# Kernel tuning notes

Hardware: AMD Instinct MI355X
Metric: run time of the kernel (lower is better)

The kernel has to match this reference:

```python
import jax, jax.numpy as jnp
import numpy as np

B, S, D, H = 2, 2048, 2048, 16
DH = D // H
NEG = -1000000000.0


def setup_inputs() -> dict:
    key = jax.random.key(0)
    ks = jax.random.split(key, 5)
    return {
        "query_vector": jax.random.normal(ks[0], (B, S, D), dtype=jnp.float32),
        "key_vector": jax.random.normal(ks[1], (B, S, D), dtype=jnp.float32),
        "value_vector": jax.random.normal(ks[2], (B, S, D), dtype=jnp.float32),
        "W_qkv": jax.random.normal(ks[3], (D, 3 * D), dtype=jnp.float32) * (1.0 / np.sqrt(D)),
        "b_qkv": jax.random.normal(ks[4], (3 * D,), dtype=jnp.float32) * 0.01,
    }


def reference(query_vector, key_vector, value_vector, W_qkv, b_qkv):
    # NOTE: original forward only consumes query_vector; key/value args unused.
    qkv = query_vector @ W_qkv + b_qkv                      # [B, S, 3D]
    q, k, v = jnp.split(qkv, 3, axis=-1)                    # each [B, S, D]
    # Faithful to original: plain reshape (NOT transpose) into heads.
    q = q.reshape(B, H, S, DH)
    k = k.reshape(B, H, S, DH)
    v = v.reshape(B, H, S, DH)
    scores = jnp.einsum("bhqd,bhkd->bhqk", q, k) / np.float32(np.sqrt(DH))
    # torch.triu_indices(offset=0): mask j >= i (diagonal included), SET to -1e9.
    idx = jnp.arange(S)
    causal = idx[None, :] >= idx[:, None]                   # [S, S], True where masked
    scores = jnp.where(causal, jnp.float32(NEG), scores)
    attn = jax.nn.softmax(scores, axis=-1)
    out = jnp.einsum("bhqk,bhkd->bhqd", attn, v)            # [B, H, S, DH]
    # dropout is identity in eval mode
    return out.reshape(B, S, D)
```

## Files before the change

kernel.cpp:

```cpp
#include <hip/hip_runtime.h>
#include <hip/hip_bf16.h>
#include <stdint.h>

typedef unsigned short u16;
typedef short short8 __attribute__((ext_vector_type(8)));
typedef short short4v __attribute__((ext_vector_type(4)));
typedef float f32x4 __attribute__((ext_vector_type(4)));

#define CSL (0.08838834764831845f * 1.4426950408889634f)
#define NEGR -1.0e13f


__device__ __forceinline__ u16 f2b(float f) {
  union { float f; unsigned int u; } c; c.f = f;
  unsigned int u = c.u;
  u += 0x7fffu + ((u >> 16) & 1u);
  return (u16)(u >> 16);
}
__device__ __forceinline__ float b2f(u16 h) {
  union { float f; unsigned int u; } c; c.u = ((unsigned int)h) << 16;
  return c.f;
}

__global__ __launch_bounds__(256) void k_cast_q(const float* __restrict__ in, u16* __restrict__ out) {
  size_t idx = ((size_t)blockIdx.x * 256 + threadIdx.x) * 8;
  float4 f0 = *(const float4*)(in + idx);
  float4 f1 = *(const float4*)(in + idx + 4);
  short8 o;
  o[0] = (short)f2b(f0.x); o[1] = (short)f2b(f0.y); o[2] = (short)f2b(f0.z); o[3] = (short)f2b(f0.w);
  o[4] = (short)f2b(f1.x); o[5] = (short)f2b(f1.y); o[6] = (short)f2b(f1.z); o[7] = (short)f2b(f1.w);
  *(short8*)(out + idx) = o;
}

__global__ __launch_bounds__(256) void k_cast_wt(const float* __restrict__ W, u16* __restrict__ Wt) {
  __shared__ u16 L[64 * 68];
  const int t = threadIdx.x;
  const int nb = blockIdx.x * 64;
  const int kb = blockIdx.y * 64;
#pragma unroll
  for (int it = 0; it < 4; ++it) {
    int idx = it * 1024 + t * 4;
    int r = idx >> 6, c = idx & 63;
    float4 f = *(const float4*)(W + (size_t)(kb + r) * 6144 + nb + c);
    L[r * 68 + c + 0] = f2b(f.x);
    L[r * 68 + c + 1] = f2b(f.y);
    L[r * 68 + c + 2] = f2b(f.z);
    L[r * 68 + c + 3] = f2b(f.w);
  }
  __syncthreads();
#pragma unroll
  for (int it = 0; it < 4; ++it) {
    int idx = it * 1024 + t * 4;
    int i = idx >> 6, j = idx & 63;
    short4v o;
#pragma unroll
    for (int e = 0; e < 4; ++e) o[e] = (short)L[(j + e) * 68 + i];
    *(short4v*)(Wt + (size_t)(nb + i) * 2048 + kb + j) = o;
  }
}

__global__ __launch_bounds__(512, 1) void k_gemm256(const u16* __restrict__ A,
                                                    const u16* __restrict__ Bt,
                                                    const float* __restrict__ bias,
                                                    u16* __restrict__ qb,
                                                    u16* __restrict__ kbuf,
                                                    u16* __restrict__ vbuf) {
  __shared__ u16 As[2][16384];
  __shared__ u16 Bs[2][12288];
  const int t = threadIdx.x;
  const int ln = t & 63, w = t >> 6;
  const int lr = ln & 15, lg = ln >> 4;
  const int wm = w >> 2, wn = w & 3;
  const int Lid = blockIdx.x;
  const int xcd = Lid & 7, l = Lid >> 3;
  const int mt = (xcd & 1) * 8 + (l & 7);
  const int nt = (xcd >> 1) * 8 + (l >> 3);
  const int mb = mt * 256, nb = nt * 192;
  const int cswz = (lr & 7) * 8;
  const int srow = w * 8 + (ln >> 3);
  const int scol = ((ln & 7) ^ (ln >> 3)) * 8;

  const u16* Abase = A + (size_t)mb * 2048;
  const u16* Bbase = Bt + (size_t)nb * 2048;

  f32x4 acc[8][3] = {};

#define STAGE_KT(kt_, buf_)                                                                        \
  do {                                                                                             \
    const u16* as_ = Abase + (size_t)srow * 2048 + (kt_) * 64 + scol;                              \
    const u16* bs_ = Bbase + (size_t)srow * 2048 + (kt_) * 64 + scol;                              \
    _Pragma("unroll")                                                                              \
    for (int p = 0; p < 4; ++p)                                                                    \
      __builtin_amdgcn_global_load_lds(                                                            \
          (const __attribute__((address_space(1))) void*)(as_ + (size_t)p * 64 * 2048),            \
          (__attribute__((address_space(3))) void*)(&As[buf_][p * 4096 + w * 512]), 16, 0, 0);     \
    _Pragma("unroll")                                                                              \
    for (int p = 0; p < 3; ++p)                                                                    \
      __builtin_amdgcn_global_load_lds(                                                            \
          (const __attribute__((address_space(1))) void*)(bs_ + (size_t)p * 64 * 2048),            \
          (__attribute__((address_space(3))) void*)(&Bs[buf_][p * 4096 + w * 512]), 16, 0, 0);     \
  } while (0)

  STAGE_KT(0, 0);
  asm volatile("s_waitcnt vmcnt(0)" ::: "memory");
  __builtin_amdgcn_s_barrier();

  for (int kt = 0; kt < 32; ++kt) {
    const int cur = kt & 1;
    const u16* At = &As[cur][0];
    const u16* Bl = &Bs[cur][0];
    short8 af[4][2], bf[3][2];

#pragma unroll
    for (int mi = 0; mi < 4; ++mi)
#pragma unroll
      for (int ks = 0; ks < 2; ++ks)
        af[mi][ks] = *(const short8*)(At + (wm * 128 + mi * 16 + lr) * 64 + ((ks * 32 + lg * 8) ^ cswz));
#pragma unroll
    for (int ni = 0; ni < 3; ++ni)
#pragma unroll
      for (int ks = 0; ks < 2; ++ks)
        bf[ni][ks] = *(const short8*)(Bl + (wn * 48 + ni * 16 + lr) * 64 + ((ks * 32 + lg * 8) ^ cswz));
    if (kt + 1 < 32) STAGE_KT(kt + 1, cur ^ 1);
    __builtin_amdgcn_s_barrier();
    __builtin_amdgcn_s_setprio(1);
#pragma unroll
    for (int mi = 0; mi < 4; ++mi)
#pragma unroll
      for (int ni = 0; ni < 3; ++ni)
#pragma unroll
        for (int ks = 0; ks < 2; ++ks)
          acc[mi][ni] = __builtin_amdgcn_mfma_f32_16x16x32_bf16(af[mi][ks], bf[ni][ks], acc[mi][ni], 0, 0, 0);
    __builtin_amdgcn_s_setprio(0);
    __builtin_amdgcn_s_barrier();

#pragma unroll
    for (int mi = 0; mi < 4; ++mi)
#pragma unroll
      for (int ks = 0; ks < 2; ++ks)
        af[mi][ks] = *(const short8*)(At + (wm * 128 + 64 + mi * 16 + lr) * 64 + ((ks * 32 + lg * 8) ^ cswz));
    __builtin_amdgcn_s_barrier();
    __builtin_amdgcn_s_setprio(1);
#pragma unroll
    for (int mi = 0; mi < 4; ++mi)
#pragma unroll
      for (int ni = 0; ni < 3; ++ni)
#pragma unroll
        for (int ks = 0; ks < 2; ++ks)
          acc[4 + mi][ni] = __builtin_amdgcn_mfma_f32_16x16x32_bf16(af[mi][ks], bf[ni][ks], acc[4 + mi][ni], 0, 0, 0);
    __builtin_amdgcn_s_setprio(0);
    asm volatile("s_waitcnt vmcnt(0)" ::: "memory");
    __builtin_amdgcn_s_barrier();
  }
#undef STAGE_KT

#pragma unroll
  for (int ni = 0; ni < 3; ++ni) {
    int ncol = nb + wn * 48 + ni * 16 + lr;
    u16* dst = (ncol < 2048) ? qb : (ncol < 4096 ? kbuf : vbuf);
    int nmod = ncol & 2047;
    float bv = bias[ncol];
#pragma unroll
    for (int m = 0; m < 8; ++m) {
#pragma unroll
      for (int r = 0; r < 4; ++r) {
        int mrow = mb + wm * 128 + m * 16 + lg * 4 + r;
        dst[(size_t)mrow * 2048 + nmod] = f2b(acc[m][ni][r] + bv);
      }
    }
  }
}

__global__ __launch_bounds__(256) void k_vtrans(const u16* __restrict__ v, u16* __restrict__ vt,
                                                float* __restrict__ part) {
  __shared__ u16 L[128 * 136];
  __shared__ float Ls2[256];
  const int t = threadIdx.x;
  const int bh = blockIdx.y, sc = blockIdx.x;
  const size_t base = (size_t)bh * 262144;
#pragma unroll
  for (int it = 0; it < 8; ++it) {
    int chunk = it * 256 + t;
    int s = chunk >> 4, d8 = (chunk & 15) * 8;
    *(short8*)(L + s * 136 + d8) = *(const short8*)(v + base + (size_t)(sc * 128 + s) * 128 + d8);
  }
  __syncthreads();
#pragma unroll
  for (int it = 0; it < 8; ++it) {
    int chunk = it * 256 + t;
    int dh = chunk >> 4, s8 = (chunk & 15) * 8;
    short8 o;
#pragma unroll
    for (int e = 0; e < 8; ++e) o[e] = (short)L[(s8 + e) * 136 + dh];
    *(short8*)(vt + base + (size_t)dh * 2048 + sc * 128 + s8) = o;
  }
  {
    const int dh = t & 127, seg = t >> 7;
    float ps = 0.f;
#pragma unroll 8
    for (int i = 0; i < 64; ++i) ps += b2f(L[(seg * 64 + i) * 136 + dh]);
    Ls2[t] = ps;
    __syncthreads();
    if (t < 128) part[((size_t)bh * 16 + sc) * 128 + t] = Ls2[t] + Ls2[t + 128];
  }
}

__global__ __launch_bounds__(256, 3) void k_attn(const u16* __restrict__ qb,
                                                 const u16* __restrict__ kb,
                                                 const u16* __restrict__ vt,
                                                 const float* __restrict__ part,
                                                 float* __restrict__ out) {
  __shared__ u16 Ks[64 * 136];
  __shared__ u16 Vs[128 * 72];
  __shared__ u16 Ps[4][16 * 72];
  const int t = threadIdx.x;
  const int ln = t & 63, wv = t >> 6;
  const int lr = ln & 15, lg = ln >> 4;
  const int L = blockIdx.y * 32 + blockIdx.x;
  const int wl = (L & 7) * 128 + (L >> 3);
  const int bh = wl >> 5;
  const int qt = 31 - (wl & 31);
  const size_t base = (size_t)bh * 262144;
  const u16* Qh = qb + base;
  const u16* Kh = kb + base;
  const u16* Vth = vt + base;
  float* Oh = out + base;
  const int qs = qt * 64;

  short8 qf[4];
  {
    int qr = qs + wv * 16 + lr;
#pragma unroll
    for (int ks = 0; ks < 4; ++ks)
      qf[ks] = *(const short8*)(Qh + (size_t)qr * 128 + ks * 32 + lg * 8);
  }
  float lsum[4] = {0.f, 0.f, 0.f, 0.f};
  f32x4 acc[8];
  const f32x4 fz = {0.f, 0.f, 0.f, 0.f};
#pragma unroll
  for (int oj = 0; oj < 8; ++oj) acc[oj] = fz;

  u16* Pw = &Ps[wv][0];
  const int nkt = qt + 1;
  for (int kt = 0; kt < nkt; ++kt) {
#pragma unroll
    for (int it = 0; it < 4; ++it) {
      int chunk = it * 256 + t;
      int sk = chunk >> 4, d8 = (chunk & 15) * 8;
      *(short8*)(Ks + sk * 136 + d8) = *(const short8*)(Kh + (size_t)(kt * 64 + sk) * 128 + d8);
    }
#pragma unroll
    for (int it = 0; it < 4; ++it) {
      int chunk = it * 256 + t;
      int dh = chunk >> 3, s8 = (chunk & 7) * 8;
      *(short8*)(Vs + dh * 72 + s8) = *(const short8*)(Vth + (size_t)dh * 2048 + kt * 64 + s8);
    }
    __syncthreads();

    f32x4 s[4];
#pragma unroll
    for (int ni = 0; ni < 4; ++ni) s[ni] = fz;
#pragma unroll
    for (int ks = 0; ks < 4; ++ks) {
#pragma unroll
      for (int ni = 0; ni < 4; ++ni) {
        short8 kf = *(const short8*)(Ks + (ni * 16 + lr) * 136 + ks * 32 + lg * 8);
        s[ni] = __builtin_amdgcn_mfma_f32_16x16x32_bf16(qf[ks], kf, s[ni], 0, 0, 0);
      }
    }
    if (kt == qt) {
#pragma unroll
      for (int ni = 0; ni < 4; ++ni) {
        int col = kt * 64 + ni * 16 + lr;
#pragma unroll
        for (int r = 0; r < 4; ++r) {
          int row = qs + wv * 16 + lg * 4 + r;
          if (col >= row) s[ni][r] = NEGR;
        }
      }
    }
#pragma unroll
    for (int ni = 0; ni < 4; ++ni)
#pragma unroll
      for (int r = 0; r < 4; ++r) {
        u16 h = f2b(exp2f(s[ni][r] * CSL));
        Pw[(lg * 4 + r) * 72 + ni * 16 + lr] = h;
        lsum[r] += b2f(h);
      }
#pragma unroll
    for (int ks2 = 0; ks2 < 2; ++ks2) {
      short8 pa = *(const short8*)(Pw + lr * 72 + ks2 * 32 + lg * 8);
#pragma unroll
      for (int oj = 0; oj < 8; ++oj) {
        short8 vf = *(const short8*)(Vs + (oj * 16 + lr) * 72 + ks2 * 32 + lg * 8);
        acc[oj] = __builtin_amdgcn_mfma_f32_16x16x32_bf16(pa, vf, acc[oj], 0, 0, 0);
      }
    }
    __syncthreads();
  }

  float rl[4];
#pragma unroll
  for (int r = 0; r < 4; ++r) {
    float sa = lsum[r];
#pragma unroll
    for (int d = 1; d < 16; d <<= 1) sa += __shfl_xor(sa, d, 64);
    rl[r] = 1.0f / sa;
  }
#pragma unroll
  for (int oj = 0; oj < 8; ++oj)
#pragma unroll
    for (int r = 0; r < 4; ++r) {
      int row = qs + wv * 16 + lg * 4 + r;
      float val = acc[oj][r] * rl[r];
      if (qt == 0 && wv == 0 && lg == 0 && r == 0) {
        float vs = 0.f;
#pragma unroll
        for (int sc = 0; sc < 16; ++sc) vs += part[(size_t)bh * 2048 + sc * 128 + oj * 16 + lr];
        val = vs * (1.0f / 2048.0f);
      }
      Oh[(size_t)row * 128 + oj * 16 + lr] = val;
    }
}

extern "C" void kernel_launch(void* const* d_in, const int* in_sizes, int n_in,
                              void* d_out, int out_size, void* d_ws, size_t ws_size,
                              hipStream_t stream) {
  (void)in_sizes; (void)n_in; (void)out_size; (void)ws_size;
  const float* q_in = (const float*)d_in[0];
  const float* W = (const float*)d_in[3];
  const float* bias = (const float*)d_in[4];
  float* out = (float*)d_out;

  u16* qbf = (u16*)d_ws;
  u16* wtb = qbf + (size_t)4096 * 2048;
  u16* qb  = wtb + (size_t)6144 * 2048;
  u16* kbf = qb  + (size_t)4096 * 2048;
  u16* vbf = kbf + (size_t)4096 * 2048;
  u16* vt  = vbf + (size_t)4096 * 2048;
  float* part = (float*)(vt + (size_t)4096 * 2048);

  k_cast_q<<<4096, 256, 0, stream>>>(q_in, qbf);
  k_cast_wt<<<dim3(96, 32), 256, 0, stream>>>(W, wtb);
  k_gemm256<<<512, 512, 0, stream>>>(qbf, wtb, bias, qb, kbf, vbf);
  k_vtrans<<<dim3(16, 32), 256, 0, stream>>>(vbf, vt, part);
  k_attn<<<dim3(32, 32), 256, 0, stream>>>(qb, kbf, vt, part, out);
}
```

Before: 230.6 us.

## Split QKV GEMM tile prefetch into two stages with partial vmcnt waits

The next k-tile's global-to-LDS loads in the QKV projection GEMM are split into two groups, issued before each of the two MFMA half-phases. The full vmcnt(0) wait at the end of each iteration becomes partial waits (vmcnt(2), vmcnt(5)), so loads stay in flight across compute. On the last iteration it prefetches a wrapped-around tile that is never used, which adds wasted traffic, and the partial waits depend on exact load counts to stay correct.

```diff
diff --git a/kernel.cpp b/kernel.cpp
--- a/kernel.cpp
+++ b/kernel.cpp
@@ -85,15 +85,16 @@
 
   f32x4 acc[8][3] = {};
 
-#define STAGE_KT(kt_, buf_)                                                                        \
+#define STAGE_S1(kt_, buf_)                                                                        \
   do {                                                                                             \
     const u16* as_ = Abase + (size_t)srow * 2048 + (kt_) * 64 + scol;                              \
     const u16* bs_ = Bbase + (size_t)srow * 2048 + (kt_) * 64 + scol;                              \
-    _Pragma("unroll")                                                                              \
-    for (int p = 0; p < 4; ++p)                                                                    \
-      __builtin_amdgcn_global_load_lds(                                                            \
-          (const __attribute__((address_space(1))) void*)(as_ + (size_t)p * 64 * 2048),            \
-          (__attribute__((address_space(3))) void*)(&As[buf_][p * 4096 + w * 512]), 16, 0, 0);     \
+    __builtin_amdgcn_global_load_lds(                                                              \
+        (const __attribute__((address_space(1))) void*)(as_),                                      \
+        (__attribute__((address_space(3))) void*)(&As[buf_][0 * 4096 + w * 512]), 16, 0, 0);       \
+    __builtin_amdgcn_global_load_lds(                                                              \
+        (const __attribute__((address_space(1))) void*)(as_ + (size_t)2 * 64 * 2048),              \
+        (__attribute__((address_space(3))) void*)(&As[buf_][2 * 4096 + w * 512]), 16, 0, 0);       \
     _Pragma("unroll")                                                                              \
     for (int p = 0; p < 3; ++p)                                                                    \
       __builtin_amdgcn_global_load_lds(                                                            \
@@ -101,16 +102,31 @@
           (__attribute__((address_space(3))) void*)(&Bs[buf_][p * 4096 + w * 512]), 16, 0, 0);     \
   } while (0)
 
-  STAGE_KT(0, 0);
+#define STAGE_S2(kt_, buf_)                                                                        \
+  do {                                                                                             \
+    const u16* as_ = Abase + (size_t)srow * 2048 + (kt_) * 64 + scol;                              \
+    __builtin_amdgcn_global_load_lds(                                                              \
+        (const __attribute__((address_space(1))) void*)(as_ + (size_t)1 * 64 * 2048),              \
+        (__attribute__((address_space(3))) void*)(&As[buf_][1 * 4096 + w * 512]), 16, 0, 0);       \
+    __builtin_amdgcn_global_load_lds(                                                              \
+        (const __attribute__((address_space(1))) void*)(as_ + (size_t)3 * 64 * 2048),              \
+        (__attribute__((address_space(3))) void*)(&As[buf_][3 * 4096 + w * 512]), 16, 0, 0);       \
+  } while (0)
+
+  STAGE_S1(0, 0);
+  STAGE_S2(0, 0);
   asm volatile("s_waitcnt vmcnt(0)" ::: "memory");
   __builtin_amdgcn_s_barrier();
 
   for (int kt = 0; kt < 32; ++kt) {
     const int cur = kt & 1;
+    const int ktn = (kt + 1) & 31;
     const u16* At = &As[cur][0];
     const u16* Bl = &Bs[cur][0];
     short8 af[4][2], bf[3][2];
 
+    asm volatile("s_waitcnt vmcnt(2)" ::: "memory");
+    __builtin_amdgcn_s_barrier();
 #pragma unroll
     for (int mi = 0; mi < 4; ++mi)
 #pragma unroll
@@ -121,7 +137,7 @@
 #pragma unroll
       for (int ks = 0; ks < 2; ++ks)
         bf[ni][ks] = *(const short8*)(Bl + (wn * 48 + ni * 16 + lr) * 64 + ((ks * 32 + lg * 8) ^ cswz));
-    if (kt + 1 < 32) STAGE_KT(kt + 1, cur ^ 1);
+    STAGE_S1(ktn, cur ^ 1);
     __builtin_amdgcn_s_barrier();
     __builtin_amdgcn_s_setprio(1);
 #pragma unroll
@@ -132,13 +148,15 @@
         for (int ks = 0; ks < 2; ++ks)
           acc[mi][ni] = __builtin_amdgcn_mfma_f32_16x16x32_bf16(af[mi][ks], bf[ni][ks], acc[mi][ni], 0, 0, 0);
     __builtin_amdgcn_s_setprio(0);
+
+    asm volatile("s_waitcnt vmcnt(5)" ::: "memory");
     __builtin_amdgcn_s_barrier();
-
 #pragma unroll
     for (int mi = 0; mi < 4; ++mi)
 #pragma unroll
       for (int ks = 0; ks < 2; ++ks)
         af[mi][ks] = *(const short8*)(At + (wm * 128 + 64 + mi * 16 + lr) * 64 + ((ks * 32 + lg * 8) ^ cswz));
+    STAGE_S2(ktn, cur ^ 1);
     __builtin_amdgcn_s_barrier();
     __builtin_amdgcn_s_setprio(1);
 #pragma unroll
@@ -149,10 +167,10 @@
         for (int ks = 0; ks < 2; ++ks)
           acc[4 + mi][ni] = __builtin_amdgcn_mfma_f32_16x16x32_bf16(af[mi][ks], bf[ni][ks], acc[4 + mi][ni], 0, 0, 0);
     __builtin_amdgcn_s_setprio(0);
-    asm volatile("s_waitcnt vmcnt(0)" ::: "memory");
-    __builtin_amdgcn_s_barrier();
-  }
-#undef STAGE_KT
+  }
+#undef STAGE_S1
+#undef STAGE_S2
+  asm volatile("s_waitcnt vmcnt(0)" ::: "memory");
 
 #pragma unroll
   for (int ni = 0; ni < 3; ++ni) {
```

After: 227.0 us. No clear change (-1.6%).
